# Kernel tuning notes

Hardware: AMD Instinct MI355X
Metric: run time of the kernel (lower is better)

Reference implementation:

```python
import jax, jax.numpy as jnp
import numpy as np

N_NODES = 20000
N_EDGES = 320000
D_IN = 256
DIMS = [512, 256, 128]
NEG_SLOPE = 0.2


def gatv2(x, src, dst, Wl, Wr, att, b, n):
    # GATv2Conv (heads=1, no self loops, no edge_attr)
    xl = x @ Wl                      # [N, D] source transform (lin_l)
    xr = x @ Wr                      # [N, D] target transform (lin_r)
    e = jax.nn.leaky_relu(xl[src] + xr[dst], NEG_SLOPE) @ att  # [E]
    # segment softmax over destination nodes
    m = jax.ops.segment_max(e, dst, num_segments=n)
    ex = jnp.exp(e - m[dst])
    s = jax.ops.segment_sum(ex, dst, num_segments=n)
    alpha = ex / (s[dst] + 1e-16)
    out = jax.ops.segment_sum(alpha[:, None] * xl[src], dst, num_segments=n)
    return out + b


def setup_inputs() -> dict:
    key = jax.random.key(0)
    ks = jax.random.split(key, 32)
    x = jax.random.normal(ks[0], (N_NODES, D_IN), dtype=jnp.float32)
    edge_index = jax.random.randint(ks[1], (2, N_EDGES), 0, N_NODES, dtype=jnp.int32)
    inp = {"x": x, "edge_index": edge_index}
    d_in = D_IN
    ki = 2
    for li, d_out in enumerate(DIMS, start=1):
        sc = 1.0 / np.sqrt(d_in)
        inp[f"Wl{li}"] = jax.random.normal(ks[ki + 0], (d_in, d_out), dtype=jnp.float32) * sc
        inp[f"Wr{li}"] = jax.random.normal(ks[ki + 1], (d_in, d_out), dtype=jnp.float32) * sc
        inp[f"att{li}"] = jax.random.normal(ks[ki + 2], (d_out,), dtype=jnp.float32) * (1.0 / np.sqrt(d_out))
        inp[f"bc{li}"] = jnp.zeros((d_out,), dtype=jnp.float32)
        inp[f"Ws{li}"] = jax.random.normal(ks[ki + 3], (d_in, d_out), dtype=jnp.float32) * sc
        inp[f"bs{li}"] = jnp.zeros((d_out,), dtype=jnp.float32)
        ki += 4
        d_in = d_out
    return inp


def reference(x, edge_index,
              Wl1, Wr1, att1, bc1, Ws1, bs1,
              Wl2, Wr2, att2, bc2, Ws2, bs2,
              Wl3, Wr3, att3, bc3, Ws3, bs3):
    src, dst = edge_index[0], edge_index[1]
    n = x.shape[0]
    h = gatv2(x, src, dst, Wl1, Wr1, att1, bc1, n) + (x @ Ws1 + bs1)
    h = jax.nn.relu(h)
    h = gatv2(h, src, dst, Wl2, Wr2, att2, bc2, n) + (h @ Ws2 + bs2)
    h = jax.nn.relu(h)
    h = gatv2(h, src, dst, Wl3, Wr3, att3, bc3, n) + (h @ Ws3 + bs3)
    return h
```

## Files before the change

kernel.cpp:

```cpp
#include <hip/hip_runtime.h>
#include <hip/hip_bf16.h>
#include <math.h>

#define N_NODES 20000
#define N_EDGES 320000

typedef _Float16 f16x8 __attribute__((ext_vector_type(8)));
typedef _Float16 h2 __attribute__((ext_vector_type(2)));
typedef float f32x4 __attribute__((ext_vector_type(4)));

__device__ __forceinline__ unsigned short f2h_bits(float f) {
    _Float16 h = (_Float16)f;
    return __builtin_bit_cast(unsigned short, h);
}

typedef const unsigned int __attribute__((address_space(1)))* gas_ptr;
typedef unsigned int __attribute__((address_space(3)))* las_ptr;
__device__ __forceinline__ void gld16(const unsigned short* g, unsigned short* l) {
    __builtin_amdgcn_global_load_lds((gas_ptr)(const void*)g, (las_ptr)(void*)l, 16, 0, 0);
}

__global__ void zero_int_kernel(int* __restrict__ p, int n) {
    int i = blockIdx.x * blockDim.x + threadIdx.x;
    if (i < n) p[i] = 0;
}

__global__ void count_deg_kernel(const int* __restrict__ dst, int* __restrict__ deg, int E) {
    int i = blockIdx.x * blockDim.x + threadIdx.x;
    if (i < E) atomicAdd(&deg[dst[i]], 1);
}

#define SCAN_T 1024
#define SCAN_C 20
__global__ __launch_bounds__(1024) void scan_kernel(const int* __restrict__ deg,
                                                    int* __restrict__ offs,
                                                    int* __restrict__ cursor, int n) {
    __shared__ int sd[SCAN_T];
    int t = threadIdx.x;
    int base = t * SCAN_C;
    int vex[SCAN_C];
    int run = 0;
#pragma unroll
    for (int k = 0; k < SCAN_C; ++k) {
        int i = base + k;
        int d = (i < n) ? deg[i] : 0;
        vex[k] = run;
        run += d;
    }
    sd[t] = run;
    __syncthreads();
    for (int off = 1; off < SCAN_T; off <<= 1) {
        int x = (t >= off) ? sd[t - off] : 0;
        __syncthreads();
        sd[t] += x;
        __syncthreads();
    }
    int excl = sd[t] - run;
#pragma unroll
    for (int k = 0; k < SCAN_C; ++k) {
        int i = base + k;
        if (i < n) { int e = excl + vex[k]; offs[i] = e; cursor[i] = e; }
    }
    if (t == SCAN_T - 1) offs[n] = sd[t];
}

__global__ void scatter_kernel(const int* __restrict__ src, const int* __restrict__ dst,
                               int* __restrict__ cursor, int* __restrict__ csr_src, int E) {
    int i = blockIdx.x * blockDim.x + threadIdx.x;
    if (i < E) {
        int pos = atomicAdd(&cursor[dst[i]], 1);
        csr_src[pos] = src[i];
    }
}

struct PrepJobs {
    const float* W[9];
    unsigned short* Wt[9];
    int K[9];
    int D[9];
    int tbeg[10];
    const float* x;
    unsigned short* xh;
    int nconv4;
};
__global__ __launch_bounds__(256) void prep_kernel(PrepJobs jb) {
    int bid = blockIdx.x;
    int ntile = jb.tbeg[9];
    if (bid < ntile) {
        __shared__ float ld[32][33];
        int job = 0;
        while (bid >= jb.tbeg[job + 1]) ++job;
        int tl = bid - jb.tbeg[job];
        int K = jb.K[job], D = jb.D[job];
        int TK = K >> 5;
        int td = tl / TK, tk = tl - td * TK;
        int k0 = tk << 5, d0 = td << 5;
        int t = threadIdx.x;
        int c = t & 31, r0 = (t >> 5) << 2;
        const float* Wp = jb.W[job];
#pragma unroll
        for (int jj = 0; jj < 4; ++jj)
            ld[r0 + jj][c] = Wp[(size_t)(k0 + r0 + jj) * D + d0 + c];
        __syncthreads();
        unsigned short* Wtp = jb.Wt[job];
#pragma unroll
        for (int jj = 0; jj < 4; ++jj) {
            int dr = r0 + jj;
            Wtp[(size_t)(d0 + dr) * K + k0 + c] = f2h_bits(ld[c][dr]);
        }
    } else {
        int cidx = (bid - ntile) * 256 + (int)threadIdx.x;
        if (cidx < jb.nconv4) {
            int base = cidx * 4;
            float4 v = *(const float4*)(jb.x + base);
            uint2 pk;
            pk.x = (unsigned int)f2h_bits(v.x) | ((unsigned int)f2h_bits(v.y) << 16);
            pk.y = (unsigned int)f2h_bits(v.z) | ((unsigned int)f2h_bits(v.w) << 16);
            *(uint2*)(jb.xh + base) = pk;
        }
    }
}

template <int SEED_F32>
__global__ __launch_bounds__(256) void gemm3_kernel(
        const unsigned short* __restrict__ A,
        const unsigned short* __restrict__ Bt,
        unsigned short* __restrict__ xlh,
        unsigned short* __restrict__ xrh,
        unsigned short* __restrict__ seedh,
        float* __restrict__ seedf,
        const float* __restrict__ b1,
        const float* __restrict__ b2,
        int M, int K, int D) {
    __shared__ __align__(16) unsigned short Asl[128 * 64];
    __shared__ __align__(16) unsigned short Bsl[128 * 64];

    int NC = (3 * D) >> 7;
    int MT = (M + 127) >> 7;
    int g = blockIdx.x;
    int xcd = g & 7, slot = g >> 3;
    int m_local = slot / NC, c = slot - m_local * NC;
    int mt = m_local * 8 + xcd;
    if (mt >= MT) return;

    int tid = threadIdx.x;
    int wave = tid >> 6, lane = tid & 63;
    int q = lane >> 4, t = lane & 15;
    int wm = (wave & 1) * 64, wn = (wave >> 1) * 64;
    int bm = mt << 7;
    int bn_all = c << 7;
    int seg = bn_all / D;
    int bn = bn_all - seg * D;

    f32x4 acc[4][4];
#pragma unroll
    for (int i = 0; i < 4; ++i)
#pragma unroll
        for (int j = 0; j < 4; ++j) acc[i][j] = (f32x4){0.f, 0.f, 0.f, 0.f};

    for (int k0 = 0; k0 < K; k0 += 64) {
#pragma unroll
        for (int rnd = 0; rnd < 4; ++rnd) {
            int ch = rnd * 256 + tid;
            int row = ch >> 3, part = ch & 7;
            int gr = bm + row; if (gr >= M) gr = M - 1;
            gld16(A + (size_t)gr * K + k0 + part * 8,
                  Asl + (rnd * 256 + wave * 64) * 8);
        }
#pragma unroll
        for (int rnd = 0; rnd < 4; ++rnd) {
            int ch = rnd * 256 + tid;
            int row = ch >> 3, part = ch & 7;
            gld16(Bt + (size_t)(bn_all + row) * K + k0 + part * 8,
                  Bsl + (rnd * 256 + wave * 64) * 8);
        }
        __syncthreads();

#pragma unroll
        for (int kk = 0; kk < 2; ++kk) {
            f16x8 an[4], am[4];
#pragma unroll
            for (int jn = 0; jn < 4; ++jn)
                an[jn] = *(const f16x8*)(Bsl + (wn + jn * 16 + t) * 64 + kk * 32 + q * 8);
#pragma unroll
            for (int im = 0; im < 4; ++im)
                am[im] = *(const f16x8*)(Asl + (wm + im * 16 + t) * 64 + kk * 32 + q * 8);
#pragma unroll
            for (int jn = 0; jn < 4; ++jn)
#pragma unroll
                for (int im = 0; im < 4; ++im)
                    acc[jn][im] = __builtin_amdgcn_mfma_f32_16x16x32_f16(an[jn], am[im], acc[jn][im], 0, 0, 0);
        }
        __syncthreads();
    }

#pragma unroll
    for (int jn = 0; jn < 4; ++jn) {
        int n0 = bn + wn + jn * 16 + q * 4;
        float bx = 0.f, by = 0.f, bz = 0.f, bw = 0.f;
        if (seg == 2) {
            float4 bb1 = *(const float4*)(b1 + n0);
            float4 bb2 = *(const float4*)(b2 + n0);
            bx = bb1.x + bb2.x; by = bb1.y + bb2.y;
            bz = bb1.z + bb2.z; bw = bb1.w + bb2.w;
        }
#pragma unroll
        for (int im = 0; im < 4; ++im) {
            int m = bm + wm + im * 16 + t;
            if (m < M) {
                float v0 = acc[jn][im][0] + bx;
                float v1 = acc[jn][im][1] + by;
                float v2 = acc[jn][im][2] + bz;
                float v3 = acc[jn][im][3] + bw;
                size_t idx = (size_t)m * D + n0;
                if (seg == 2 && SEED_F32) {
                    *(float4*)(seedf + idx) = make_float4(v0, v1, v2, v3);
                } else {
                    uint2 pk;
                    pk.x = (unsigned int)f2h_bits(v0) | ((unsigned int)f2h_bits(v1) << 16);
                    pk.y = (unsigned int)f2h_bits(v2) | ((unsigned int)f2h_bits(v3) << 16);
                    unsigned short* dstp = (seg == 0) ? xlh : (seg == 1) ? xrh : seedh;
                    *(uint2*)(dstp + idx) = pk;
                }
            }
        }
    }
}

template <int D, int SEED_H, int WRITE_H, int RELU>
__global__ __launch_bounds__(128) void fused_agg_kernel(
        const unsigned short* __restrict__ xl,
        const unsigned short* __restrict__ xr,
        const float* __restrict__ att,
        const int* __restrict__ offs,
        const int* __restrict__ csr_src,
        const unsigned short* __restrict__ seedh,
        const float* __restrict__ seedf,
        float* __restrict__ outf,
        unsigned short* __restrict__ outh) {
    constexpr int VPL = D / 64;
    constexpr int HP = VPL / 2;
    typedef _Float16 hvec __attribute__((ext_vector_type(VPL)));

    int wave = threadIdx.x >> 6, lane = threadIdx.x & 63;
    int n = blockIdx.x * 2 + wave;
    if (n >= N_NODES) return;
    int beg = offs[n], end = offs[n + 1];

    h2 xr_h[HP], att_h[HP];
    hvec xrv = *(const hvec*)(xr + (size_t)n * D + lane * VPL);
#pragma unroll
    for (int pp = 0; pp < HP; ++pp) {
        xr_h[pp] = (h2){xrv[2 * pp], xrv[2 * pp + 1]};
        att_h[pp] = (h2){(_Float16)att[lane * VPL + 2 * pp],
                         (_Float16)att[lane * VPL + 2 * pp + 1]};
    }

    float acc[VPL];
#pragma unroll
    for (int v = 0; v < VPL; ++v) acc[v] = 0.f;
    float m = -INFINITY, s = 0.f;

    const _Float16 c02 = (_Float16)0.2f;
    int lb0 = lane & 1;
    int lb1 = lane & 2;

    int nfull = (end - beg) >> 2;
    int j = beg;
    int i0 = 0, i1 = 0, i2 = 0, i3 = 0;
    if (nfull > 0) {
        i0 = csr_src[beg]; i1 = csr_src[beg + 1];
        i2 = csr_src[beg + 2]; i3 = csr_src[beg + 3];
    }
    for (int b = 0; b < nfull; ++b) {
        int s0 = i0, s1 = i1, s2 = i2, s3 = i3;
        int jn4 = j + 4;
        if (b + 1 < nfull) {
            i0 = csr_src[jn4]; i1 = csr_src[jn4 + 1];
            i2 = csr_src[jn4 + 2]; i3 = csr_src[jn4 + 3];
        }
        hvec x0 = *(const hvec*)(xl + (size_t)s0 * D + lane * VPL);
        hvec x1 = *(const hvec*)(xl + (size_t)s1 * D + lane * VPL);
        hvec x2 = *(const hvec*)(xl + (size_t)s2 * D + lane * VPL);
        hvec x3 = *(const hvec*)(xl + (size_t)s3 * D + lane * VPL);
        float p0 = 0.f, p1 = 0.f, p2 = 0.f, p3 = 0.f;
#pragma unroll
        for (int pp = 0; pp < HP; ++pp) {
            h2 a0 = (h2){x0[2 * pp], x0[2 * pp + 1]};
            h2 a1 = (h2){x1[2 * pp], x1[2 * pp + 1]};
            h2 a2 = (h2){x2[2 * pp], x2[2 * pp + 1]};
            h2 a3 = (h2){x3[2 * pp], x3[2 * pp + 1]};
            h2 z0 = a0 + xr_h[pp];
            h2 z1 = a1 + xr_h[pp];
            h2 z2 = a2 + xr_h[pp];
            h2 z3 = a3 + xr_h[pp];
            h2 l0 = __builtin_elementwise_max(z0, z0 * c02);
            h2 l1 = __builtin_elementwise_max(z1, z1 * c02);
            h2 l2 = __builtin_elementwise_max(z2, z2 * c02);
            h2 l3 = __builtin_elementwise_max(z3, z3 * c02);
#if __has_builtin(__builtin_amdgcn_fdot2)
            p0 = __builtin_amdgcn_fdot2(l0, att_h[pp], p0, false);
            p1 = __builtin_amdgcn_fdot2(l1, att_h[pp], p1, false);
            p2 = __builtin_amdgcn_fdot2(l2, att_h[pp], p2, false);
            p3 = __builtin_amdgcn_fdot2(l3, att_h[pp], p3, false);
#else
            p0 += (float)l0.x * (float)att_h[pp].x + (float)l0.y * (float)att_h[pp].y;
            p1 += (float)l1.x * (float)att_h[pp].x + (float)l1.y * (float)att_h[pp].y;
            p2 += (float)l2.x * (float)att_h[pp].x + (float)l2.y * (float)att_h[pp].y;
            p3 += (float)l3.x * (float)att_h[pp].x + (float)l3.y * (float)att_h[pp].y;
#endif
        }
        float k0 = lb0 ? p1 : p0, sn0 = lb0 ? p0 : p1;
        float k1 = lb0 ? p3 : p2, sn1 = lb0 ? p2 : p3;
        k0 += __shfl_xor(sn0, 1, 64);
        k1 += __shfl_xor(sn1, 1, 64);
        float k = lb1 ? k1 : k0, sn = lb1 ? k0 : k1;
        k += __shfl_xor(sn, 2, 64);
        k += __shfl_xor(k, 4, 64);
        k += __shfl_xor(k, 8, 64);
        k += __shfl_xor(k, 16, 64);
        k += __shfl_xor(k, 32, 64);
        float q0 = __shfl(k, 0, 64);
        float q1 = __shfl(k, 1, 64);
        float q2 = __shfl(k, 2, 64);
        float q3 = __shfl(k, 3, 64);

        float mn = fmaxf(m, fmaxf(fmaxf(q0, q1), fmaxf(q2, q3)));
        float sc = __expf(m - mn);
        float e0 = __expf(q0 - mn);
        float e1 = __expf(q1 - mn);
        float e2 = __expf(q2 - mn);
        float e3 = __expf(q3 - mn);
        s = s * sc + e0 + e1 + e2 + e3;
#pragma unroll
        for (int v = 0; v < VPL; ++v)
            acc[v] = acc[v] * sc + e0 * (float)x0[v] + e1 * (float)x1[v]
                                 + e2 * (float)x2[v] + e3 * (float)x3[v];
        m = mn;
        j = jn4;
    }
    for (; j < end; ++j) {
        int s0 = csr_src[j];
        hvec x0 = *(const hvec*)(xl + (size_t)s0 * D + lane * VPL);
        float p0 = 0.f;
#pragma unroll
        for (int pp = 0; pp < HP; ++pp) {
            h2 a0 = (h2){x0[2 * pp], x0[2 * pp + 1]};
            h2 z0 = a0 + xr_h[pp];
            h2 l0 = __builtin_elementwise_max(z0, z0 * c02);
#if __has_builtin(__builtin_amdgcn_fdot2)
            p0 = __builtin_amdgcn_fdot2(l0, att_h[pp], p0, false);
#else
            p0 += (float)l0.x * (float)att_h[pp].x + (float)l0.y * (float)att_h[pp].y;
#endif
        }
#pragma unroll
        for (int o = 32; o > 0; o >>= 1) p0 += __shfl_xor(p0, o, 64);
        float mn = fmaxf(m, p0);
        float sc = __expf(m - mn);
        float e0 = __expf(p0 - mn);
        s = s * sc + e0;
#pragma unroll
        for (int v = 0; v < VPL; ++v) acc[v] = acc[v] * sc + e0 * (float)x0[v];
        m = mn;
    }

    float sinv = 1.0f / (s + 1e-16f);
    size_t base = (size_t)n * D + lane * VPL;
    float sd[VPL];
    if (SEED_H) {
        hvec sv = *(const hvec*)(seedh + base);
#pragma unroll
        for (int v = 0; v < VPL; ++v) sd[v] = (float)sv[v];
    } else {
#pragma unroll
        for (int v = 0; v < VPL; ++v) sd[v] = seedf[base + v];
    }
#pragma unroll
    for (int v = 0; v < VPL; ++v) {
        float val = sd[v] + acc[v] * sinv;
        if (RELU) val = fmaxf(val, 0.f);
        if (WRITE_H) outh[base + v] = f2h_bits(val);
        else         outf[base + v] = val;
    }
}

static void run_layer(const unsigned short* hact, int K, int D,
                      const unsigned short* Wcat,
                      const float* att, const float* bc, const float* bs,
                      unsigned short* xlh, unsigned short* xrh,
                      unsigned short* seedh, float* seedf,
                      const int* offs, const int* csr_src,
                      float* outf, unsigned short* outh, int final_layer,
                      hipStream_t stream) {
    int NC = 3 * D / 128;
    int MT = (N_NODES + 127) / 128;
    int nblk = 8 * ((MT + 7) / 8) * NC;
    if (final_layer)
        hipLaunchKernelGGL((gemm3_kernel<1>), dim3(nblk), dim3(256), 0, stream, hact, Wcat,
                           xlh, xrh, (unsigned short*)nullptr, seedf, bs, bc, N_NODES, K, D);
    else
        hipLaunchKernelGGL((gemm3_kernel<0>), dim3(nblk), dim3(256), 0, stream, hact, Wcat,
                           xlh, xrh, seedh, (float*)nullptr, bs, bc, N_NODES, K, D);

    dim3 agrid((N_NODES + 1) / 2);
    if (D == 512) {
        hipLaunchKernelGGL((fused_agg_kernel<512, 1, 1, 1>), agrid, dim3(128), 0, stream,
                           xlh, xrh, att, offs, csr_src, seedh, (const float*)nullptr,
                           (float*)nullptr, outh);
    } else if (D == 256) {
        hipLaunchKernelGGL((fused_agg_kernel<256, 1, 1, 1>), agrid, dim3(128), 0, stream,
                           xlh, xrh, att, offs, csr_src, seedh, (const float*)nullptr,
                           (float*)nullptr, outh);
    } else {
        hipLaunchKernelGGL((fused_agg_kernel<128, 0, 0, 0>), agrid, dim3(128), 0, stream,
                           xlh, xrh, att, offs, csr_src, (const unsigned short*)nullptr, seedf,
                           outf, (unsigned short*)nullptr);
    }
}

extern "C" void kernel_launch(void* const* d_in, const int* in_sizes, int n_in,
                              void* d_out, int out_size, void* d_ws, size_t ws_size,
                              hipStream_t stream) {
    const float* x = (const float*)d_in[0];
    const int* ei = (const int*)d_in[1];
    const int* src = ei;
    const int* dst = ei + N_EDGES;

    const float* Wl1 = (const float*)d_in[2];
    const float* Wr1 = (const float*)d_in[3];
    const float* att1 = (const float*)d_in[4];
    const float* bc1 = (const float*)d_in[5];
    const float* Ws1 = (const float*)d_in[6];
    const float* bs1 = (const float*)d_in[7];
    const float* Wl2 = (const float*)d_in[8];
    const float* Wr2 = (const float*)d_in[9];
    const float* att2 = (const float*)d_in[10];
    const float* bc2 = (const float*)d_in[11];
    const float* Ws2 = (const float*)d_in[12];
    const float* bs2 = (const float*)d_in[13];
    const float* Wl3 = (const float*)d_in[14];
    const float* Wr3 = (const float*)d_in[15];
    const float* att3 = (const float*)d_in[16];
    const float* bc3 = (const float*)d_in[17];
    const float* Ws3 = (const float*)d_in[18];
    const float* bs3 = (const float*)d_in[19];

    const size_t NF = (size_t)N_NODES * 512;
    const size_t NH = (size_t)N_NODES * 256;
    unsigned short* xlh   = (unsigned short*)d_ws;
    unsigned short* xrh   = xlh + NF;
    unsigned short* seedh = xrh + NF;
    unsigned short* xhf   = seedh + NF;
    unsigned short* h1h   = xhf + NH;
    unsigned short* h2h   = h1h + NF;
    unsigned short* Wcat1 = h2h + NH;
    unsigned short* Wcat2 = Wcat1 + 3 * 512 * 256;
    unsigned short* Wcat3 = Wcat2 + 3 * 256 * 512;
    int* deg     = (int*)(Wcat3 + 3 * 128 * 256);
    int* offs    = deg + N_NODES;
    int* cursor  = offs + N_NODES + 1;
    int* csr_src = cursor + N_NODES;
    size_t needed = (size_t)((char*)(csr_src + N_EDGES) - (char*)d_ws);
    if (ws_size < needed) return;

    hipLaunchKernelGGL(zero_int_kernel, dim3((N_NODES + 255) / 256), dim3(256), 0, stream,
                       deg, N_NODES);
    hipLaunchKernelGGL(count_deg_kernel, dim3((N_EDGES + 255) / 256), dim3(256), 0, stream,
                       dst, deg, N_EDGES);
    hipLaunchKernelGGL(scan_kernel, dim3(1), dim3(SCAN_T), 0, stream, deg, offs, cursor, N_NODES);
    hipLaunchKernelGGL(scatter_kernel, dim3((N_EDGES + 255) / 256), dim3(256), 0, stream,
                       src, dst, cursor, csr_src, N_EDGES);

    {
        PrepJobs jb;
        const float* Ws_[9]  = {Wl1, Wr1, Ws1, Wl2, Wr2, Ws2, Wl3, Wr3, Ws3};
        unsigned short* Wt_[9] = {Wcat1, Wcat1 + 512 * 256, Wcat1 + 2 * 512 * 256,
                                  Wcat2, Wcat2 + 256 * 512, Wcat2 + 2 * 256 * 512,
                                  Wcat3, Wcat3 + 128 * 256, Wcat3 + 2 * 128 * 256};
        int K_[9] = {256, 256, 256, 512, 512, 512, 256, 256, 256};
        int D_[9] = {512, 512, 512, 256, 256, 256, 128, 128, 128};
        int o = 0;
        for (int i = 0; i < 9; ++i) {
            jb.W[i] = Ws_[i]; jb.Wt[i] = Wt_[i]; jb.K[i] = K_[i]; jb.D[i] = D_[i];
            jb.tbeg[i] = o; o += (K_[i] >> 5) * (D_[i] >> 5);
        }
        jb.tbeg[9] = o;
        jb.x = x;
        jb.xh = xhf;
        jb.nconv4 = N_NODES * 256 / 4;
        int nconv_blocks = (jb.nconv4 + 255) / 256;
        hipLaunchKernelGGL(prep_kernel, dim3(o + nconv_blocks), dim3(256), 0, stream, jb);
    }

    run_layer(xhf, 256, 512, Wcat1, att1, bc1, bs1,
              xlh, xrh, seedh, (float*)nullptr, offs, csr_src,
              (float*)nullptr, h1h, 0, stream);
    run_layer(h1h, 512, 256, Wcat2, att2, bc2, bs2,
              xlh, xrh, seedh, (float*)nullptr, offs, csr_src,
              (float*)nullptr, h2h, 0, stream);
    run_layer(h2h, 256, 128, Wcat3, att3, bc3, bs3,
              xlh, xrh, (unsigned short*)nullptr, (float*)d_out, offs, csr_src,
              (float*)d_out, (unsigned short*)nullptr, 1, stream);
}
```

Baseline: 364.2 us.

## Fuse CSR build and weight prep into one cooperative setup kernel

Replaces the five setup launches (zero degrees, count, single-block scan, scatter, weight transpose/convert) with one cooperative kernel of 256 blocks that uses grid-wide syncs between phases. The scan becomes a two-level, multi-block scan with a per-block partials array. Weight transposes and the x conversion now overlap with the degree-counting phase. This removes launch overheads and the serial single-block scan, at the cost of several grid barriers and fewer blocks (256) for the atomic and transpose work.

Measured after the change: 623.2 us. 1.71x slower.

```diff
diff --git a/kernel.cpp b/kernel.cpp
--- a/kernel.cpp
+++ b/kernel.cpp
@@ -1,6 +1,9 @@
 #include <hip/hip_runtime.h>
 #include <hip/hip_bf16.h>
+#include <hip/hip_cooperative_groups.h>
 #include <math.h>
+
+namespace cg = cooperative_groups;
 
 #define N_NODES 20000
 #define N_EDGES 320000
@@ -20,60 +23,7 @@
     __builtin_amdgcn_global_load_lds((gas_ptr)(const void*)g, (las_ptr)(void*)l, 16, 0, 0);
 }
 
-__global__ void zero_int_kernel(int* __restrict__ p, int n) {
-    int i = blockIdx.x * blockDim.x + threadIdx.x;
-    if (i < n) p[i] = 0;
-}
-
-__global__ void count_deg_kernel(const int* __restrict__ dst, int* __restrict__ deg, int E) {
-    int i = blockIdx.x * blockDim.x + threadIdx.x;
-    if (i < E) atomicAdd(&deg[dst[i]], 1);
-}
-
-#define SCAN_T 1024
-#define SCAN_C 20
-__global__ __launch_bounds__(1024) void scan_kernel(const int* __restrict__ deg,
-                                                    int* __restrict__ offs,
-                                                    int* __restrict__ cursor, int n) {
-    __shared__ int sd[SCAN_T];
-    int t = threadIdx.x;
-    int base = t * SCAN_C;
-    int vex[SCAN_C];
-    int run = 0;
-#pragma unroll
-    for (int k = 0; k < SCAN_C; ++k) {
-        int i = base + k;
-        int d = (i < n) ? deg[i] : 0;
-        vex[k] = run;
-        run += d;
-    }
-    sd[t] = run;
-    __syncthreads();
-    for (int off = 1; off < SCAN_T; off <<= 1) {
-        int x = (t >= off) ? sd[t - off] : 0;
-        __syncthreads();
-        sd[t] += x;
-        __syncthreads();
-    }
-    int excl = sd[t] - run;
-#pragma unroll
-    for (int k = 0; k < SCAN_C; ++k) {
-        int i = base + k;
-        if (i < n) { int e = excl + vex[k]; offs[i] = e; cursor[i] = e; }
-    }
-    if (t == SCAN_T - 1) offs[n] = sd[t];
-}
-
-__global__ void scatter_kernel(const int* __restrict__ src, const int* __restrict__ dst,
-                               int* __restrict__ cursor, int* __restrict__ csr_src, int E) {
-    int i = blockIdx.x * blockDim.x + threadIdx.x;
-    if (i < E) {
-        int pos = atomicAdd(&cursor[dst[i]], 1);
-        csr_src[pos] = src[i];
-    }
-}
-
-struct PrepJobs {
+struct SetupArgs {
     const float* W[9];
     unsigned short* Wt[9];
     int K[9];
@@ -82,42 +32,118 @@
     const float* x;
     unsigned short* xh;
     int nconv4;
+    const int* src;
+    const int* dst;
+    int* deg;
+    int* offs;
+    int* cursor;
+    int* csr_src;
+    int* partial;
 };
-__global__ __launch_bounds__(256) void prep_kernel(PrepJobs jb) {
-    int bid = blockIdx.x;
-    int ntile = jb.tbeg[9];
-    if (bid < ntile) {
-        __shared__ float ld[32][33];
+
+#define SETUP_B 256
+#define SETUP_T 256
+#define CHUNK 79
+
+__global__ __launch_bounds__(SETUP_T) void setup_kernel(SetupArgs a) {
+    cg::grid_group grid = cg::this_grid();
+    __shared__ __align__(16) char smemraw[32 * 33 * 4];
+    float (*ld)[33] = (float(*)[33])smemraw;
+    int* sdat = (int*)smemraw;
+
+    int bid = blockIdx.x, t = threadIdx.x;
+    int gtid = bid * SETUP_T + t;
+    const int gstride = SETUP_B * SETUP_T;
+
+    for (int i = gtid; i < N_NODES; i += gstride) a.deg[i] = 0;
+    __threadfence();
+    grid.sync();
+
+    for (int i = gtid; i < N_EDGES; i += gstride) atomicAdd(&a.deg[a.dst[i]], 1);
+
+    int ntile = a.tbeg[9];
+    for (int tl0 = bid; tl0 < ntile; tl0 += SETUP_B) {
         int job = 0;
-        while (bid >= jb.tbeg[job + 1]) ++job;
-        int tl = bid - jb.tbeg[job];
-        int K = jb.K[job], D = jb.D[job];
+        while (tl0 >= a.tbeg[job + 1]) ++job;
+        int tl = tl0 - a.tbeg[job];
+        int K = a.K[job], D = a.D[job];
         int TK = K >> 5;
         int td = tl / TK, tk = tl - td * TK;
         int k0 = tk << 5, d0 = td << 5;
-        int t = threadIdx.x;
         int c = t & 31, r0 = (t >> 5) << 2;
-        const float* Wp = jb.W[job];
+        const float* Wp = a.W[job];
+        __syncthreads();
 #pragma unroll
         for (int jj = 0; jj < 4; ++jj)
             ld[r0 + jj][c] = Wp[(size_t)(k0 + r0 + jj) * D + d0 + c];
         __syncthreads();
-        unsigned short* Wtp = jb.Wt[job];
+        unsigned short* Wtp = a.Wt[job];
 #pragma unroll
         for (int jj = 0; jj < 4; ++jj) {
             int dr = r0 + jj;
             Wtp[(size_t)(d0 + dr) * K + k0 + c] = f2h_bits(ld[c][dr]);
         }
-    } else {
-        int cidx = (bid - ntile) * 256 + (int)threadIdx.x;
-        if (cidx < jb.nconv4) {
-            int base = cidx * 4;
-            float4 v = *(const float4*)(jb.x + base);
-            uint2 pk;
-            pk.x = (unsigned int)f2h_bits(v.x) | ((unsigned int)f2h_bits(v.y) << 16);
-            pk.y = (unsigned int)f2h_bits(v.z) | ((unsigned int)f2h_bits(v.w) << 16);
-            *(uint2*)(jb.xh + base) = pk;
-        }
+    }
+
+    for (int cdx = gtid; cdx < a.nconv4; cdx += gstride) {
+        int base = cdx * 4;
+        float4 v = *(const float4*)(a.x + base);
+        uint2 pk;
+        pk.x = (unsigned int)f2h_bits(v.x) | ((unsigned int)f2h_bits(v.y) << 16);
+        pk.y = (unsigned int)f2h_bits(v.z) | ((unsigned int)f2h_bits(v.w) << 16);
+        *(uint2*)(a.xh + base) = pk;
+    }
+    __threadfence();
+    grid.sync();
+
+    __syncthreads();
+    int base = bid * CHUNK;
+    int v = 0;
+    if (t < CHUNK && base + t < N_NODES) v = a.deg[base + t];
+    sdat[t] = v;
+    __syncthreads();
+    for (int off = 1; off < SETUP_T; off <<= 1) {
+        int x2 = (t >= off) ? sdat[t - off] : 0;
+        __syncthreads();
+        sdat[t] += x2;
+        __syncthreads();
+    }
+    int incl = sdat[t];
+    if (t == SETUP_T - 1) a.partial[bid] = incl;
+    __threadfence();
+    grid.sync();
+
+    if (bid == 0) {
+        int p = a.partial[t];
+        __syncthreads();
+        sdat[t] = p;
+        __syncthreads();
+        for (int off = 1; off < SETUP_T; off <<= 1) {
+            int x2 = (t >= off) ? sdat[t - off] : 0;
+            __syncthreads();
+            sdat[t] += x2;
+            __syncthreads();
+        }
+        a.partial[t] = sdat[t] - p;
+        __threadfence();
+    }
+    grid.sync();
+
+    {
+        int bx = a.partial[bid];
+        if (t < CHUNK && base + t < N_NODES) {
+            int e = bx + incl - v;
+            a.offs[base + t] = e;
+            a.cursor[base + t] = e;
+        }
+        if (gtid == 0) a.offs[N_NODES] = N_EDGES;
+    }
+    __threadfence();
+    grid.sync();
+
+    for (int i = gtid; i < N_EDGES; i += gstride) {
+        int pos = atomicAdd(&a.cursor[a.dst[i]], 1);
+        a.csr_src[pos] = a.src[i];
     }
 }
 
@@ -461,19 +487,12 @@
     int* offs    = deg + N_NODES;
     int* cursor  = offs + N_NODES + 1;
     int* csr_src = cursor + N_NODES;
-    size_t needed = (size_t)((char*)(csr_src + N_EDGES) - (char*)d_ws);
+    int* partial = csr_src + N_EDGES;
+    size_t needed = (size_t)((char*)(partial + 256) - (char*)d_ws);
     if (ws_size < needed) return;
 
-    hipLaunchKernelGGL(zero_int_kernel, dim3((N_NODES + 255) / 256), dim3(256), 0, stream,
-                       deg, N_NODES);
-    hipLaunchKernelGGL(count_deg_kernel, dim3((N_EDGES + 255) / 256), dim3(256), 0, stream,
-                       dst, deg, N_EDGES);
-    hipLaunchKernelGGL(scan_kernel, dim3(1), dim3(SCAN_T), 0, stream, deg, offs, cursor, N_NODES);
-    hipLaunchKernelGGL(scatter_kernel, dim3((N_EDGES + 255) / 256), dim3(256), 0, stream,
-                       src, dst, cursor, csr_src, N_EDGES);
-
     {
-        PrepJobs jb;
+        SetupArgs sa;
         const float* Ws_[9]  = {Wl1, Wr1, Ws1, Wl2, Wr2, Ws2, Wl3, Wr3, Ws3};
         unsigned short* Wt_[9] = {Wcat1, Wcat1 + 512 * 256, Wcat1 + 2 * 512 * 256,
                                   Wcat2, Wcat2 + 256 * 512, Wcat2 + 2 * 256 * 512,
@@ -482,15 +501,23 @@
         int D_[9] = {512, 512, 512, 256, 256, 256, 128, 128, 128};
         int o = 0;
         for (int i = 0; i < 9; ++i) {
-            jb.W[i] = Ws_[i]; jb.Wt[i] = Wt_[i]; jb.K[i] = K_[i]; jb.D[i] = D_[i];
-            jb.tbeg[i] = o; o += (K_[i] >> 5) * (D_[i] >> 5);
-        }
-        jb.tbeg[9] = o;
-        jb.x = x;
-        jb.xh = xhf;
-        jb.nconv4 = N_NODES * 256 / 4;
-        int nconv_blocks = (jb.nconv4 + 255) / 256;
-        hipLaunchKernelGGL(prep_kernel, dim3(o + nconv_blocks), dim3(256), 0, stream, jb);
+            sa.W[i] = Ws_[i]; sa.Wt[i] = Wt_[i]; sa.K[i] = K_[i]; sa.D[i] = D_[i];
+            sa.tbeg[i] = o; o += (K_[i] >> 5) * (D_[i] >> 5);
+        }
+        sa.tbeg[9] = o;
+        sa.x = x;
+        sa.xh = xhf;
+        sa.nconv4 = N_NODES * 256 / 4;
+        sa.src = src;
+        sa.dst = dst;
+        sa.deg = deg;
+        sa.offs = offs;
+        sa.cursor = cursor;
+        sa.csr_src = csr_src;
+        sa.partial = partial;
+        void* args[] = { &sa };
+        hipLaunchCooperativeKernel((void*)setup_kernel, dim3(SETUP_B), dim3(SETUP_T),
+                                   args, 0, stream);
     }
 
     run_layer(xhf, 256, 512, Wcat1, att1, bc1, bs1,
```
